# Optimization experiments

Hardware: AMD Instinct MI355X
Metric: run time of the kernel (lower is better)

The kernel has to match this reference:

```python
import jax, jax.numpy as jnp
import numpy as np

N = 4096
VOCAB = 50257
EDIM = 1024
WFEAT = 1024
LABELS = 2
SLOPE = 0.01
NEG_INF = -1e9


def setup_inputs() -> dict:
    key = jax.random.key(0)
    ks = jax.random.split(key, 8)
    inSen = jax.random.randint(ks[0], (N,), 0, VOCAB, dtype=jnp.int64)
    adj = jax.random.randint(ks[1], (N, N), 0, 2, dtype=jnp.int32)
    emb_table = jax.random.normal(ks[2], (VOCAB, EDIM), dtype=jnp.float32) * 0.02
    W = jax.random.normal(ks[3], (EDIM, WFEAT), dtype=jnp.float32) * (1.0 / np.sqrt(EDIM))
    a_src = jax.random.normal(ks[4], (WFEAT,), dtype=jnp.float32) * (1.0 / np.sqrt(WFEAT))
    a_dst = jax.random.normal(ks[5], (WFEAT,), dtype=jnp.float32) * (1.0 / np.sqrt(WFEAT))
    clf_w = jax.random.normal(ks[6], (WFEAT, LABELS), dtype=jnp.float32) * (1.0 / np.sqrt(WFEAT))
    clf_b = jax.random.normal(ks[7], (LABELS,), dtype=jnp.float32) * 0.01
    return {"inSen": inSen, "adj": adj, "emb_table": emb_table, "W": W,
            "a_src": a_src, "a_dst": a_dst, "clf_w": clf_w, "clf_b": clf_b}


def reference(inSen, adj, emb_table, W, a_src, a_dst, clf_w, clf_b):
    # Embedding lookup: [N, edim]
    words = emb_table[inSen]
    # GAT layer: linear projection [N, wFeat]
    h = words @ W
    # Pairwise attention logits e_ij = LeakyReLU(a_src.h_i + a_dst.h_j)
    s_src = h @ a_src            # [N]
    s_dst = h @ a_dst            # [N]
    e = jax.nn.leaky_relu(s_src[:, None] + s_dst[None, :], negative_slope=SLOPE)  # [N, N]
    # Adjacency-masked softmax over neighbors (axis=1)
    e = jnp.where(adj > 0, e, NEG_INF)
    attention = jax.nn.softmax(e, axis=1)          # [N, N]
    sentence = attention @ h                       # [N, wFeat]
    # Mean pooling over nodes
    poolSentence = jnp.mean(sentence, axis=0)      # [wFeat]
    # Classifier + softmax over labels (dim=0 of a 1-D vector)
    label = jax.nn.softmax(poolSentence @ clf_w + clf_b, axis=0)  # [labels]
    return (poolSentence, attention, sentence, label)
```

## Files before the change

kernel.cpp:

```cpp
#include <hip/hip_runtime.h>
#include <hip/hip_bf16.h>

#define NN 4096
#define ED 1024
#define WF 1024
#define SLOPEC 0.01f
#define NEG_INFC -1e9f

typedef __attribute__((ext_vector_type(8))) short bf16x8;
typedef __attribute__((ext_vector_type(4))) short short4v;
typedef __attribute__((ext_vector_type(4))) float f32x4;

__device__ __forceinline__ float bf2f(short s) {
    union { unsigned u; float f; } v;
    v.u = ((unsigned)(unsigned short)s) << 16;
    return v.f;
}
__device__ __forceinline__ short f2bf(float f) {
    unsigned u = __float_as_uint(f);
    unsigned r = u + 0x7FFFu + ((u >> 16) & 1u);
    return (short)(r >> 16);
}

typedef __attribute__((address_space(3))) unsigned lds_u32;
typedef const __attribute__((address_space(1))) unsigned gbl_u32;
__device__ __forceinline__ void g2l16(const short* g, short* l) {
    __builtin_amdgcn_global_load_lds((gbl_u32*)g, (lds_u32*)l, 16, 0, 0);
}

__global__ __launch_bounds__(256) void k_wt(const float* __restrict__ W,
                                            short* __restrict__ Wt) {
    __shared__ float t[64][65];
    const int k0 = blockIdx.y * 64, n0 = blockIdx.x * 64;
    const int tx = threadIdx.x & 63, ty = threadIdx.x >> 6;
#pragma unroll
    for (int p = 0; p < 16; p++) {
        int r = p * 4 + ty;
        t[r][tx] = W[(long)(k0 + r) * WF + n0 + tx];
    }
    __syncthreads();
#pragma unroll
    for (int p = 0; p < 16; p++) {
        int r = p * 4 + ty;
        Wt[(long)(n0 + r) * ED + k0 + tx] = f2bf(t[tx][r]);
    }
}

__global__ __launch_bounds__(256) void k_gather(const int* __restrict__ inSen,
                                                const float* __restrict__ emb,
                                                short* __restrict__ X) {
    const int row = blockIdx.x;
    const int tid = threadIdx.x;
    const long idx = inSen[row];
    const float4 v = ((const float4*)(emb + idx * ED))[tid];
    short4v s;
    s.x = f2bf(v.x); s.y = f2bf(v.y); s.z = f2bf(v.z); s.w = f2bf(v.w);
    *(short4v*)(X + (long)row * ED + tid * 4) = s;
}

template <bool ATOMIC_OUT>
__global__ __launch_bounds__(256, 2) void gemm_bt2(
    const short* __restrict__ A, const short* __restrict__ Bt,
    int M, int N, int K, int Kc, float* __restrict__ Cout) {
    __shared__ __align__(16) short sA[128 * 32];
    __shared__ __align__(16) short sB[128 * 32];

    const int tid = threadIdx.x;
    const int lane = tid & 63;
    const int wid = tid >> 6;
    const int wm = wid >> 1, wn = wid & 1;
    const int n0 = blockIdx.x * 128;
    const int m0 = blockIdx.y * 128;
    const int ks = blockIdx.z * Kc;

    const int srow = tid >> 2;
    const int sc8 = (tid & 3) * 8;
    const int l15 = lane & 15;
    const int lhi = lane >> 4;

    f32x4 acc[4][4];
#pragma unroll
    for (int t = 0; t < 4; t++)
#pragma unroll
        for (int u = 0; u < 4; u++) acc[t][u] = (f32x4){0.f, 0.f, 0.f, 0.f};

    const short* Ab = A + (long)(m0 + srow) * K + ks + sc8;
    const short* Bb = Bt + (long)(n0 + srow) * K + ks + sc8;
    short* lA0 = sA + (long)(wid * 64) * 8;
    short* lA1 = sA + (long)(256 + wid * 64) * 8;
    short* lB0 = sB + (long)(wid * 64) * 8;
    short* lB1 = sB + (long)(256 + wid * 64) * 8;
    const long rstep = (long)64 * K;

    for (int k0 = 0; k0 < Kc; k0 += 32) {
        g2l16(Ab + k0, lA0);
        g2l16(Ab + rstep + k0, lA1);
        g2l16(Bb + k0, lB0);
        g2l16(Bb + rstep + k0, lB1);
        __syncthreads();

        bf16x8 af[4], bfr[4];
#pragma unroll
        for (int t = 0; t < 4; t++)
            af[t] = *(const bf16x8*)&sA[(wm * 64 + t * 16 + l15) * 32 + lhi * 8];
#pragma unroll
        for (int u = 0; u < 4; u++)
            bfr[u] = *(const bf16x8*)&sB[(wn * 64 + u * 16 + l15) * 32 + lhi * 8];
#pragma unroll
        for (int t = 0; t < 4; t++)
#pragma unroll
            for (int u = 0; u < 4; u++)
                acc[t][u] = __builtin_amdgcn_mfma_f32_16x16x32_bf16(
                    af[t], bfr[u], acc[t][u], 0, 0, 0);
        __syncthreads();
    }

    if (ATOMIC_OUT) {
#pragma unroll
        for (int t = 0; t < 4; t++)
#pragma unroll
            for (int u = 0; u < 4; u++)
#pragma unroll
                for (int r = 0; r < 4; r++) {
                    int m = wm * 64 + t * 16 + lhi * 4 + r;
                    int n = wn * 64 + u * 16 + l15;
                    atomicAdd(Cout + (long)(m0 + m) * N + n0 + n, acc[t][u][r]);
                }
    } else {
        float* P = Cout + (long)blockIdx.z * M * N;
#pragma unroll
        for (int t = 0; t < 4; t++)
#pragma unroll
            for (int u = 0; u < 4; u++)
#pragma unroll
                for (int r = 0; r < 4; r++) {
                    int m = wm * 64 + t * 16 + lhi * 4 + r;
                    int n = wn * 64 + u * 16 + l15;
                    P[(long)(m0 + m) * N + n0 + n] = acc[t][u][r];
                }
    }
}

__global__ __launch_bounds__(256) void k_reduce1(const float* __restrict__ P,
                                                 short* __restrict__ Ht) {
    const long e = ((long)blockIdx.x * 256 + threadIdx.x) * 8;
    const long MN = (long)WF * NN;
    const float4 a0 = *(const float4*)(P + e);
    const float4 a1 = *(const float4*)(P + e + 4);
    const float4 b0 = *(const float4*)(P + MN + e);
    const float4 b1 = *(const float4*)(P + MN + e + 4);
    bf16x8 o;
    o[0] = f2bf(a0.x + b0.x); o[1] = f2bf(a0.y + b0.y);
    o[2] = f2bf(a0.z + b0.z); o[3] = f2bf(a0.w + b0.w);
    o[4] = f2bf(a1.x + b1.x); o[5] = f2bf(a1.y + b1.y);
    o[6] = f2bf(a1.z + b1.z); o[7] = f2bf(a1.w + b1.w);
    *(bf16x8*)(Ht + e) = o;
}

__global__ __launch_bounds__(256) void k_scores(const short* __restrict__ Ht,
                                                const float* __restrict__ a_src,
                                                const float* __restrict__ a_dst,
                                                float* __restrict__ s_src,
                                                float* __restrict__ s_dst) {
    const int i = blockIdx.x * 256 + threadIdx.x;
    const int f0 = blockIdx.y * 256;
    float as = 0.f, ad = 0.f;
#pragma unroll 8
    for (int f = f0; f < f0 + 256; f++) {
        float hv = bf2f(Ht[(long)f * NN + i]);
        as += hv * a_src[f];
        ad += hv * a_dst[f];
    }
    atomicAdd(s_src + i, as);
    atomicAdd(s_dst + i, ad);
}

__global__ __launch_bounds__(256) void k_attn(const int* __restrict__ adj,
                                              const float* __restrict__ s_src,
                                              const float* __restrict__ s_dst,
                                              float* __restrict__ attn,
                                              short* __restrict__ attnB) {
    __shared__ float wred[4];
    __shared__ float wred2[4];
    const int row = blockIdx.x;
    const int tid = threadIdx.x;
    const float ss = s_src[row];
    const int4* adj4 = (const int4*)(adj + (long)row * NN);
    const float4* sd4 = (const float4*)s_dst;
    float v[16];
    float vmax = -3e38f;
#pragma unroll
    for (int c = 0; c < 4; c++) {
        int idx = c * 256 + tid;
        int4 a = adj4[idx];
        float4 d = sd4[idx];
        float x0 = ss + d.x; x0 = x0 > 0.f ? x0 : SLOPEC * x0; x0 = a.x > 0 ? x0 : NEG_INFC;
        float x1 = ss + d.y; x1 = x1 > 0.f ? x1 : SLOPEC * x1; x1 = a.y > 0 ? x1 : NEG_INFC;
        float x2 = ss + d.z; x2 = x2 > 0.f ? x2 : SLOPEC * x2; x2 = a.z > 0 ? x2 : NEG_INFC;
        float x3 = ss + d.w; x3 = x3 > 0.f ? x3 : SLOPEC * x3; x3 = a.w > 0 ? x3 : NEG_INFC;
        v[c * 4 + 0] = x0; v[c * 4 + 1] = x1; v[c * 4 + 2] = x2; v[c * 4 + 3] = x3;
        vmax = fmaxf(vmax, fmaxf(fmaxf(x0, x1), fmaxf(x2, x3)));
    }
#pragma unroll
    for (int off = 32; off; off >>= 1) vmax = fmaxf(vmax, __shfl_xor(vmax, off));
    if ((tid & 63) == 0) wred[tid >> 6] = vmax;
    __syncthreads();
    vmax = fmaxf(fmaxf(wred[0], wred[1]), fmaxf(wred[2], wred[3]));

    float sum = 0.f;
#pragma unroll
    for (int c = 0; c < 16; c++) {
        v[c] = __expf(v[c] - vmax);
        sum += v[c];
    }
#pragma unroll
    for (int off = 32; off; off >>= 1) sum += __shfl_xor(sum, off);
    if ((tid & 63) == 0) wred2[tid >> 6] = sum;
    __syncthreads();
    sum = wred2[0] + wred2[1] + wred2[2] + wred2[3];
    const float inv = 1.0f / sum;

    float4* o4 = (float4*)(attn + (long)row * NN);
    short4v* b4 = (short4v*)(attnB + (long)row * NN);
#pragma unroll
    for (int c = 0; c < 4; c++) {
        int idx = c * 256 + tid;
        float4 o;
        o.x = v[c * 4 + 0] * inv; o.y = v[c * 4 + 1] * inv;
        o.z = v[c * 4 + 2] * inv; o.w = v[c * 4 + 3] * inv;
        o4[idx] = o;
        short4v sb;
        sb.x = f2bf(o.x); sb.y = f2bf(o.y); sb.z = f2bf(o.z); sb.w = f2bf(o.w);
        b4[idx] = sb;
    }
}

__global__ __launch_bounds__(256) void k_pool(const float* __restrict__ sent,
                                              float* __restrict__ pool) {
    const int tid = threadIdx.x;
    const int r0 = blockIdx.x * 64;
    float4 acc = {0.f, 0.f, 0.f, 0.f};
    const float4* s4 = (const float4*)sent;
#pragma unroll 4
    for (int r = 0; r < 64; r++) {
        float4 v = s4[(long)(r0 + r) * 256 + tid];
        acc.x += v.x; acc.y += v.y; acc.z += v.z; acc.w += v.w;
    }
    atomicAdd(pool + tid * 4 + 0, acc.x);
    atomicAdd(pool + tid * 4 + 1, acc.y);
    atomicAdd(pool + tid * 4 + 2, acc.z);
    atomicAdd(pool + tid * 4 + 3, acc.w);
}

__global__ __launch_bounds__(256) void k_final(const float* __restrict__ pool_acc,
                                               const float* __restrict__ clf_w,
                                               const float* __restrict__ clf_b,
                                               float* __restrict__ out_pool,
                                               float* __restrict__ out_label) {
    __shared__ float r0[4], r1[4];
    const int tid = threadIdx.x;
    float l0 = 0.f, l1 = 0.f;
#pragma unroll
    for (int q = 0; q < 4; q++) {
        int f = q * 256 + tid;
        float p = pool_acc[f] * (1.0f / NN);
        out_pool[f] = p;
        l0 += p * clf_w[f * 2 + 0];
        l1 += p * clf_w[f * 2 + 1];
    }
#pragma unroll
    for (int off = 32; off; off >>= 1) {
        l0 += __shfl_xor(l0, off);
        l1 += __shfl_xor(l1, off);
    }
    if ((tid & 63) == 0) { r0[tid >> 6] = l0; r1[tid >> 6] = l1; }
    __syncthreads();
    if (tid == 0) {
        float L0 = r0[0] + r0[1] + r0[2] + r0[3] + clf_b[0];
        float L1 = r1[0] + r1[1] + r1[2] + r1[3] + clf_b[1];
        float m = fmaxf(L0, L1);
        float e0 = __expf(L0 - m), e1 = __expf(L1 - m);
        float s = e0 + e1;
        out_label[0] = e0 / s;
        out_label[1] = e1 / s;
    }
}

extern "C" void kernel_launch(void* const* d_in, const int* in_sizes, int n_in,
                              void* d_out, int out_size, void* d_ws,
                              size_t ws_size, hipStream_t stream) {
    const int* inSen = (const int*)d_in[0];
    const int* adj = (const int*)d_in[1];
    const float* emb = (const float*)d_in[2];
    const float* W = (const float*)d_in[3];
    const float* a_src = (const float*)d_in[4];
    const float* a_dst = (const float*)d_in[5];
    const float* clf_w = (const float*)d_in[6];
    const float* clf_b = (const float*)d_in[7];

    float* out = (float*)d_out;
    float* out_pool = out;
    float* attn = out + 1024;
    float* sentence = out + 1024 + (long)NN * NN;
    float* out_label = out + 1024 + (long)NN * NN + (long)NN * WF;

    char* ws = (char*)d_ws;
    short* X = (short*)ws;
    short* Wt = (short*)(ws + (8l << 20));
    short* Ht = (short*)(ws + (10l << 20));
    float* P1 = (float*)(ws + (18l << 20));
    short* attnB = (short*)(ws + (18l << 20));
    float* s_src = (float*)(ws + (50l << 20));
    float* s_dst = s_src + NN;
    float* pool = s_dst + NN;

    hipMemsetAsync(s_src, 0, (2 * NN + WF) * sizeof(float), stream);
    hipMemsetAsync(sentence, 0, (long)NN * WF * sizeof(float), stream);

    k_wt<<<dim3(16, 16), 256, 0, stream>>>(W, Wt);
    k_gather<<<NN, 256, 0, stream>>>(inSen, emb, X);

    gemm_bt2<false><<<dim3(NN / 128, WF / 128, 2), 256, 0, stream>>>(
        Wt, X, WF, NN, ED, ED / 2, P1);
    k_reduce1<<<(WF * NN) / (256 * 8), 256, 0, stream>>>(P1, Ht);

    k_scores<<<dim3(NN / 256, WF / 256), 256, 0, stream>>>(Ht, a_src, a_dst,
                                                           s_src, s_dst);
    k_attn<<<NN, 256, 0, stream>>>(adj, s_src, s_dst, attn, attnB);

    gemm_bt2<true><<<dim3(WF / 128, NN / 128, 4), 256, 0, stream>>>(
        attnB, Ht, NN, WF, NN, NN / 4, sentence);

    k_pool<<<NN / 64, 256, 0, stream>>>(sentence, pool);
    k_final<<<1, 256, 0, stream>>>(pool, clf_w, clf_b, out_pool, out_label);
}
```

Before: 470.5 us.

## Drop split-K reduce for first GEMM and replace atomic second GEMM with partials

The first GEMM now runs without split-K, using a 64x128 tile, and writes bf16 Ht directly through an LDS-staged coalesced store. This removes the fp32 partial buffer and the separate reduce kernel. The second GEMM uses split-K of 2 with plain partial stores instead of split-K 4 with atomics. A new reduce kernel sums the two partials into sentence and accumulates the pool, which also drops the memset of sentence and the separate pool pass. In exchange it adds extra partial-buffer traffic, and the first GEMM launches fewer blocks at a longer K.

```diff
diff --git a/kernel.cpp b/kernel.cpp
--- a/kernel.cpp
+++ b/kernel.cpp
@@ -58,19 +58,24 @@
     *(short4v*)(X + (long)row * ED + tid * 4) = s;
 }
 
-template <bool ATOMIC_OUT>
+template <int BM, int BN, bool BF16_OUT>
 __global__ __launch_bounds__(256, 2) void gemm_bt2(
     const short* __restrict__ A, const short* __restrict__ Bt,
-    int M, int N, int K, int Kc, float* __restrict__ Cout) {
-    __shared__ __align__(16) short sA[128 * 32];
-    __shared__ __align__(16) short sB[128 * 32];
+    int M, int N, int K, int Kc, void* __restrict__ Cout, long MN) {
+    constexpr int TM = BM / 32;
+    constexpr int TN = BN / 32;
+    constexpr int STAGE = BM * 32 + BN * 32;
+    constexpr int SMEMSZ = (BF16_OUT && BM * BN > STAGE) ? BM * BN : STAGE;
+    __shared__ __align__(16) short smem[SMEMSZ];
+    short* sA = smem;
+    short* sB = smem + BM * 32;
 
     const int tid = threadIdx.x;
     const int lane = tid & 63;
     const int wid = tid >> 6;
     const int wm = wid >> 1, wn = wid & 1;
-    const int n0 = blockIdx.x * 128;
-    const int m0 = blockIdx.y * 128;
+    const int n0 = blockIdx.x * BN;
+    const int m0 = blockIdx.y * BM;
     const int ks = blockIdx.z * Kc;
 
     const int srow = tid >> 2;
@@ -78,83 +83,76 @@
     const int l15 = lane & 15;
     const int lhi = lane >> 4;
 
-    f32x4 acc[4][4];
-#pragma unroll
-    for (int t = 0; t < 4; t++)
-#pragma unroll
-        for (int u = 0; u < 4; u++) acc[t][u] = (f32x4){0.f, 0.f, 0.f, 0.f};
+    f32x4 acc[TM][TN];
+#pragma unroll
+    for (int t = 0; t < TM; t++)
+#pragma unroll
+        for (int u = 0; u < TN; u++) acc[t][u] = (f32x4){0.f, 0.f, 0.f, 0.f};
 
     const short* Ab = A + (long)(m0 + srow) * K + ks + sc8;
     const short* Bb = Bt + (long)(n0 + srow) * K + ks + sc8;
-    short* lA0 = sA + (long)(wid * 64) * 8;
-    short* lA1 = sA + (long)(256 + wid * 64) * 8;
-    short* lB0 = sB + (long)(wid * 64) * 8;
-    short* lB1 = sB + (long)(256 + wid * 64) * 8;
     const long rstep = (long)64 * K;
 
     for (int k0 = 0; k0 < Kc; k0 += 32) {
-        g2l16(Ab + k0, lA0);
-        g2l16(Ab + rstep + k0, lA1);
-        g2l16(Bb + k0, lB0);
-        g2l16(Bb + rstep + k0, lB1);
+#pragma unroll
+        for (int p = 0; p < BM / 64; p++)
+            g2l16(Ab + p * rstep + k0, sA + (p * 256 + wid * 64) * 8);
+#pragma unroll
+        for (int p = 0; p < BN / 64; p++)
+            g2l16(Bb + p * rstep + k0, sB + (p * 256 + wid * 64) * 8);
         __syncthreads();
 
-        bf16x8 af[4], bfr[4];
-#pragma unroll
-        for (int t = 0; t < 4; t++)
-            af[t] = *(const bf16x8*)&sA[(wm * 64 + t * 16 + l15) * 32 + lhi * 8];
-#pragma unroll
-        for (int u = 0; u < 4; u++)
-            bfr[u] = *(const bf16x8*)&sB[(wn * 64 + u * 16 + l15) * 32 + lhi * 8];
-#pragma unroll
-        for (int t = 0; t < 4; t++)
-#pragma unroll
-            for (int u = 0; u < 4; u++)
+        bf16x8 af[TM], bfr[TN];
+#pragma unroll
+        for (int t = 0; t < TM; t++)
+            af[t] = *(const bf16x8*)&sA[(wm * (BM / 2) + t * 16 + l15) * 32 + lhi * 8];
+#pragma unroll
+        for (int u = 0; u < TN; u++)
+            bfr[u] = *(const bf16x8*)&sB[(wn * (BN / 2) + u * 16 + l15) * 32 + lhi * 8];
+#pragma unroll
+        for (int t = 0; t < TM; t++)
+#pragma unroll
+            for (int u = 0; u < TN; u++)
                 acc[t][u] = __builtin_amdgcn_mfma_f32_16x16x32_bf16(
                     af[t], bfr[u], acc[t][u], 0, 0, 0);
         __syncthreads();
     }
 
-    if (ATOMIC_OUT) {
-#pragma unroll
-        for (int t = 0; t < 4; t++)
-#pragma unroll
-            for (int u = 0; u < 4; u++)
+    if (BF16_OUT) {
+        short* sT = smem;
+#pragma unroll
+        for (int t = 0; t < TM; t++)
+#pragma unroll
+            for (int u = 0; u < TN; u++)
 #pragma unroll
                 for (int r = 0; r < 4; r++) {
-                    int m = wm * 64 + t * 16 + lhi * 4 + r;
-                    int n = wn * 64 + u * 16 + l15;
-                    atomicAdd(Cout + (long)(m0 + m) * N + n0 + n, acc[t][u][r]);
+                    int m = wm * (BM / 2) + t * 16 + lhi * 4 + r;
+                    int n = wn * (BN / 2) + u * 16 + l15;
+                    sT[m * BN + n] = f2bf(acc[t][u][r]);
                 }
+        __syncthreads();
+        short* C = (short*)Cout;
+#pragma unroll
+        for (int q = 0; q < BM * BN / 2048; q++) {
+            int idx = q * 256 + tid;
+            int row = idx / (BN / 8);
+            int c8 = (idx % (BN / 8)) * 8;
+            *(bf16x8*)(C + (long)(m0 + row) * N + n0 + c8) =
+                *(const bf16x8*)&sT[row * BN + c8];
+        }
     } else {
-        float* P = Cout + (long)blockIdx.z * M * N;
-#pragma unroll
-        for (int t = 0; t < 4; t++)
-#pragma unroll
-            for (int u = 0; u < 4; u++)
+        float* P = (float*)Cout + (long)blockIdx.z * MN;
+#pragma unroll
+        for (int t = 0; t < TM; t++)
+#pragma unroll
+            for (int u = 0; u < TN; u++)
 #pragma unroll
                 for (int r = 0; r < 4; r++) {
-                    int m = wm * 64 + t * 16 + lhi * 4 + r;
-                    int n = wn * 64 + u * 16 + l15;
+                    int m = wm * (BM / 2) + t * 16 + lhi * 4 + r;
+                    int n = wn * (BN / 2) + u * 16 + l15;
                     P[(long)(m0 + m) * N + n0 + n] = acc[t][u][r];
                 }
     }
-}
-
-__global__ __launch_bounds__(256) void k_reduce1(const float* __restrict__ P,
-                                                 short* __restrict__ Ht) {
-    const long e = ((long)blockIdx.x * 256 + threadIdx.x) * 8;
-    const long MN = (long)WF * NN;
-    const float4 a0 = *(const float4*)(P + e);
-    const float4 a1 = *(const float4*)(P + e + 4);
-    const float4 b0 = *(const float4*)(P + MN + e);
-    const float4 b1 = *(const float4*)(P + MN + e + 4);
-    bf16x8 o;
-    o[0] = f2bf(a0.x + b0.x); o[1] = f2bf(a0.y + b0.y);
-    o[2] = f2bf(a0.z + b0.z); o[3] = f2bf(a0.w + b0.w);
-    o[4] = f2bf(a1.x + b1.x); o[5] = f2bf(a1.y + b1.y);
-    o[6] = f2bf(a1.z + b1.z); o[7] = f2bf(a1.w + b1.w);
-    *(bf16x8*)(Ht + e) = o;
 }
 
 __global__ __launch_bounds__(256) void k_scores(const short* __restrict__ Ht,
@@ -235,16 +233,23 @@
     }
 }
 
-__global__ __launch_bounds__(256) void k_pool(const float* __restrict__ sent,
-                                              float* __restrict__ pool) {
-    const int tid = threadIdx.x;
-    const int r0 = blockIdx.x * 64;
+__global__ __launch_bounds__(256) void k_reduce2(const float* __restrict__ P,
+                                                 float* __restrict__ sent,
+                                                 float* __restrict__ pool) {
+    const int tid = threadIdx.x;
+    const long MN4 = (long)NN * WF / 4;
+    const float4* P0 = (const float4*)P;
+    const float4* P1 = P0 + MN4;
+    float4* s4 = (float4*)sent;
     float4 acc = {0.f, 0.f, 0.f, 0.f};
-    const float4* s4 = (const float4*)sent;
 #pragma unroll 4
-    for (int r = 0; r < 64; r++) {
-        float4 v = s4[(long)(r0 + r) * 256 + tid];
-        acc.x += v.x; acc.y += v.y; acc.z += v.z; acc.w += v.w;
+    for (int r = 0; r < 16; r++) {
+        long e = (long)(blockIdx.x * 16 + r) * 256 + tid;
+        float4 a = P0[e], b = P1[e];
+        float4 s;
+        s.x = a.x + b.x; s.y = a.y + b.y; s.z = a.z + b.z; s.w = a.w + b.w;
+        s4[e] = s;
+        acc.x += s.x; acc.y += s.y; acc.z += s.z; acc.w += s.w;
     }
     atomicAdd(pool + tid * 4 + 0, acc.x);
     atomicAdd(pool + tid * 4 + 1, acc.y);
@@ -308,29 +313,27 @@
     short* X = (short*)ws;
     short* Wt = (short*)(ws + (8l << 20));
     short* Ht = (short*)(ws + (10l << 20));
-    float* P1 = (float*)(ws + (18l << 20));
     short* attnB = (short*)(ws + (18l << 20));
-    float* s_src = (float*)(ws + (50l << 20));
+    float* P2 = (float*)(ws + (52l << 20));
+    float* s_src = (float*)(ws + (86l << 20));
     float* s_dst = s_src + NN;
     float* pool = s_dst + NN;
 
     hipMemsetAsync(s_src, 0, (2 * NN + WF) * sizeof(float), stream);
-    hipMemsetAsync(sentence, 0, (long)NN * WF * sizeof(float), stream);
 
     k_wt<<<dim3(16, 16), 256, 0, stream>>>(W, Wt);
     k_gather<<<NN, 256, 0, stream>>>(inSen, emb, X);
 
-    gemm_bt2<false><<<dim3(NN / 128, WF / 128, 2), 256, 0, stream>>>(
-        Wt, X, WF, NN, ED, ED / 2, P1);
-    k_reduce1<<<(WF * NN) / (256 * 8), 256, 0, stream>>>(P1, Ht);
+    gemm_bt2<64, 128, true><<<dim3(NN / 128, WF / 64, 1), 256, 0, stream>>>(
+        Wt, X, WF, NN, ED, ED, Ht, 0);
 
     k_scores<<<dim3(NN / 256, WF / 256), 256, 0, stream>>>(Ht, a_src, a_dst,
                                                            s_src, s_dst);
     k_attn<<<NN, 256, 0, stream>>>(adj, s_src, s_dst, attn, attnB);
 
-    gemm_bt2<true><<<dim3(WF / 128, NN / 128, 4), 256, 0, stream>>>(
-        attnB, Ht, NN, WF, NN, NN / 4, sentence);
-
-    k_pool<<<NN / 64, 256, 0, stream>>>(sentence, pool);
+    gemm_bt2<128, 128, false><<<dim3(WF / 128, NN / 128, 2), 256, 0, stream>>>(
+        attnB, Ht, NN, WF, NN, NN / 2, P2, (long)NN * WF);
+
+    k_reduce2<<<NN / 16, 256, 0, stream>>>(P2, sentence, pool);
     k_final<<<1, 256, 0, stream>>>(pool, clf_w, clf_b, out_pool, out_label);
 }
```

Measured after the change: 446.5 us. -5.1%, faster.
